# Kernel tuning notes

Measured on AMD Instinct MI355X. Metric: run time of the kernel, lower is better.

## Reference

```python
import jax, jax.numpy as jnp
import numpy as np

B, T, D_IN, D_OUT, H = 4, 2048, 768, 768, 12
HD = D_OUT // H  # 64


def setup_inputs() -> dict:
    key = jax.random.key(0)
    ks = jax.random.split(key, 6)
    s_in = 1.0 / np.sqrt(D_IN)
    s_out = 1.0 / np.sqrt(D_OUT)
    return {
        "x": jax.random.normal(ks[0], (B, T, D_IN), dtype=jnp.float32),
        "Wq": jax.random.uniform(ks[1], (D_IN, D_OUT), jnp.float32, -s_in, s_in),
        "Wk": jax.random.uniform(ks[2], (D_IN, D_OUT), jnp.float32, -s_in, s_in),
        "Wv": jax.random.uniform(ks[3], (D_IN, D_OUT), jnp.float32, -s_in, s_in),
        "Wo": jax.random.uniform(ks[4], (D_OUT, D_OUT), jnp.float32, -s_out, s_out),
        "bo": jax.random.uniform(ks[5], (D_OUT,), jnp.float32, -s_out, s_out),
    }


def reference(x, Wq, Wk, Wv, Wo, bo):
    b, t, _ = x.shape
    # QKV projections (no bias, per qkv_bias=False), split into heads: [b,h,t,hd]
    q = (x @ Wq).reshape(b, t, H, HD).transpose(0, 2, 1, 3)
    k = (x @ Wk).reshape(b, t, H, HD).transpose(0, 2, 1, 3)
    v = (x @ Wv).reshape(b, t, H, HD).transpose(0, 2, 1, 3)
    # NOTE: original calls masked_fill (non-in-place) and discards the result,
    # so NO causal mask is actually applied. Faithfully reproduce that.
    scores = jnp.einsum("bhqd,bhkd->bhqk", q, k)  # [b,h,t,t]
    attn = jax.nn.softmax(scores / jnp.sqrt(jnp.float32(HD)), axis=-1)
    # dropout p=0.0 (eval) -> identity
    ctx = jnp.einsum("bhqk,bhkd->bhqd", attn, v)  # [b,h,t,hd]
    ctx = ctx.transpose(0, 2, 1, 3).reshape(b, t, D_OUT)
    return ctx @ Wo + bo
```

## Files before the change

kernel.cpp:

```cpp
#include <hip/hip_runtime.h>
#include <hip/hip_bf16.h>
#include <stdint.h>


#define HH   12
#define TT   2048
#define DIN  768
#define DOUT 768
#define HD   64
#define BB   4
#define MTOT (BB*TT)
#define NQKV (3*DOUT)
#define QSCALE 0.1803368801111832f

typedef float  float4v  __attribute__((ext_vector_type(4)));
typedef float  float16v __attribute__((ext_vector_type(16)));
typedef __bf16 bf16x8   __attribute__((ext_vector_type(8)));
typedef short  short8v  __attribute__((ext_vector_type(8)));

#define AS1 __attribute__((address_space(1)))
#define AS3 __attribute__((address_space(3)))

static __device__ __forceinline__ void gload_lds16(const void* g, void* l) {
    __builtin_amdgcn_global_load_lds((AS1 void*)g, (AS3 void*)l, 16, 0, 0);
}

static __device__ __forceinline__ short f2bf(float f) {
    __bf16 h = (__bf16)f;
    return __builtin_bit_cast(short, h);
}

__global__ __launch_bounds__(256) void prep_kernel(const float* __restrict__ x,
                                                   const float* __restrict__ Wq,
                                                   const float* __restrict__ Wk,
                                                   const float* __restrict__ Wv,
                                                   const float* __restrict__ Wo,
                                                   short* __restrict__ Xb,
                                                   short* __restrict__ Wqkvt,
                                                   short* __restrict__ Wot) {
    __shared__ short tile[32 * 33];
    const int bz = blockIdx.z;
    if (bz == 4) {
        const int n4 = MTOT * DIN / 4;
        int i = (blockIdx.y * 24 + blockIdx.x) * 256 + threadIdx.x;
        for (; i < n4; i += 24 * 24 * 256) {
            float4 v = ((const float4*)x)[i];
            short4 o;
            o.x = f2bf(v.x); o.y = f2bf(v.y); o.z = f2bf(v.z); o.w = f2bf(v.w);
            ((short4*)Xb)[i] = o;
        }
        return;
    }
    const int bx = blockIdx.x, by = blockIdx.y;
    const float* W = (bz == 0) ? Wq : (bz == 1) ? Wk : (bz == 2) ? Wv : Wo;
    const int tx = threadIdx.x & 31, ty = threadIdx.x >> 5;
    for (int i = 0; i < 4; i++) {
        int k = by * 32 + ty + i * 8;
        tile[(ty + i * 8) * 33 + tx] = f2bf(W[(size_t)k * DOUT + bx * 32 + tx]);
    }
    __syncthreads();
    for (int i = 0; i < 4; i++) {
        int n = bx * 32 + ty + i * 8;
        int k = by * 32 + tx;
        short v = tile[tx * 33 + ty + i * 8];
        if (bz < 3) Wqkvt[(size_t)(bz * DOUT + n) * DIN + k] = v;
        else        Wot[(size_t)n * DOUT + k] = v;
    }
}

__global__ __launch_bounds__(256) void qkv_gemm_kernel(const short* __restrict__ Xb,
                                                       const short* __restrict__ Wt,
                                                       short* __restrict__ Qb,
                                                       short* __restrict__ Kb,
                                                       short* __restrict__ Vt) {
    __shared__ __align__(16) short lds[16384];
    short* ldsA = lds;
    short* ldsB = lds + 8192;
    const int t = threadIdx.x;
    const int w = t >> 6, lane = t & 63;
    const int quad = lane >> 4, l15 = lane & 15;
    const int m0 = blockIdx.x * 128, n0 = blockIdx.y * 128;
    const int wm = (w >> 1) * 64, wn = (w & 1) * 64;

    float4v acc[4][4];
    for (int i = 0; i < 4; i++)
        for (int j = 0; j < 4; j++)
            acc[i][j] = (float4v)0.0f;

    const int rA = t >> 3;
    const int cS = ((t & 7) ^ ((t >> 3) & 7)) * 8;
    const short* gA0 = Xb + (size_t)(m0 + rA) * DIN + cS;
    const short* gB0 = Wt + (size_t)(n0 + rA) * DIN + cS;

    for (int k0 = 0; k0 < DIN; k0 += 64) {
#pragma unroll
        for (int g = 0; g < 4; g++)
            gload_lds16(gA0 + (size_t)g * 32 * DIN + k0, &ldsA[(g * 256 + t) * 8]);
#pragma unroll
        for (int g = 0; g < 4; g++)
            gload_lds16(gB0 + (size_t)g * 32 * DIN + k0, &ldsB[(g * 256 + t) * 8]);
        __syncthreads();
#pragma unroll
        for (int kk = 0; kk < 2; kk++) {
            bf16x8 af[4], bfr[4];
            const int pos = ((kk * 4 + quad) ^ (l15 & 7)) * 8;
            for (int i = 0; i < 4; i++) af[i]  = *(const bf16x8*)&ldsA[(wm + i * 16 + l15) * 64 + pos];
            for (int j = 0; j < 4; j++) bfr[j] = *(const bf16x8*)&ldsB[(wn + j * 16 + l15) * 64 + pos];
            for (int i = 0; i < 4; i++)
                for (int j = 0; j < 4; j++)
                    acc[i][j] = __builtin_amdgcn_mfma_f32_16x16x32_bf16(af[i], bfr[j], acc[i][j], 0, 0, 0);
        }
        __syncthreads();
    }

    const int which = n0 / DOUT;
    if (which < 2) {
        short* ldsT = lds;
        const float sc = (which == 0) ? QSCALE : 1.0f;
        short* dst = (which == 0) ? Qb : Kb;
        const int n0sec = n0 - which * DOUT;
        for (int i = 0; i < 4; i++)
            for (int j = 0; j < 4; j++) {
                int col = wn + j * 16 + l15;
                int cx = col >> 3, co = col & 7;
                for (int r = 0; r < 4; r++) {
                    int row = wm + i * 16 + quad * 4 + r;
                    ldsT[row * 128 + ((cx ^ (row & 7)) * 8 + co)] = f2bf(acc[i][j][r] * sc);
                }
            }
        __syncthreads();
        for (int p = 0; p < 8; p++) {
            int row = p * 16 + (t >> 4);
            int cL = t & 15;
            short8v v = *(const short8v*)&ldsT[row * 128 + ((cL ^ (row & 7)) * 8)];
            int mg = m0 + row;
            int b2 = mg >> 11, tq = mg & 2047;
            int colg = n0sec + cL * 8;
            int hh = colg >> 6, d = colg & 63;
            *(short8v*)&dst[((size_t)((b2 * HH + hh) * TT + tq) << 6) + d] = v;
        }
    } else {
        short* ldsT = lds;
        const int n0r = n0 - 2 * DOUT;
        const int b = m0 >> 11, tq0 = m0 & 2047;
        for (int i = 0; i < 4; i++)
            for (int j = 0; j < 4; j++)
                for (int r = 0; r < 4; r++) {
                    int nl = wn + j * 16 + l15;
                    int ml = wm + i * 16 + quad * 4 + r;
                    int c = ml >> 3, o = ml & 7;
                    ldsT[nl * 128 + ((c ^ (nl & 7)) * 8 + o)] = f2bf(acc[i][j][r]);
                }
        __syncthreads();
        for (int p = 0; p < 8; p++) {
            int nrow = p * 16 + (t >> 4);
            int cc = t & 15;
            short8v v = *(const short8v*)&ldsT[nrow * 128 + ((cc ^ (nrow & 7)) * 8)];
            int colg = n0r + nrow;
            int hh = colg >> 6, d = colg & 63;
            *(short8v*)&Vt[(size_t)((b * HH + hh) * HD + d) * TT + tq0 + cc * 8] = v;
        }
    }
}

__global__ __launch_bounds__(256, 3) void attn_kernel(const short* __restrict__ Qb,
                                                      const short* __restrict__ Kb,
                                                      const short* __restrict__ Vt,
                                                      short* __restrict__ Ctx) {
    __shared__ __align__(16) short ldsK[2][64 * 64];
    __shared__ __align__(16) short ldsV[2][64 * 64];
    const int t = threadIdx.x;
    const int w = t >> 6, lane = t & 63;
    const int half = lane >> 5, m = lane & 31;
    const int bh = blockIdx.x;
    const int b = bh / HH, h = bh - b * HH;
    const int q0 = blockIdx.y * 128 + w * 32;

    const short* Qbase = Qb + (size_t)bh * TT * HD;
    const short* Kbase = Kb + (size_t)bh * TT * HD;
    const short* Vbase = Vt + (size_t)bh * HD * TT;

    bf16x8 qf[4];
#pragma unroll
    for (int s = 0; s < 4; s++)
        qf[s] = *(const bf16x8*)&Qbase[(q0 + m) * HD + s * 16 + half * 8];

    int kOff[2], vOff[2];
    {
        int r5 = t >> 3;
        int pi = ((r5 >> 3) & 1) * 16 + ((r5 >> 2) & 1) * 8 + ((r5 >> 4) & 1) * 4 + (r5 & 3);
#pragma unroll
        for (int g = 0; g < 2; g++) {
            kOff[g] = (g * 32 + pi) * 64 + (((t & 7) ^ (r5 & 7)) * 8);
            int vrow = g * 32 + r5;
            vOff[g] = vrow * TT + (((t & 7) ^ (vrow & 7)) * 8);
        }
    }

    auto stage = [&](int buf, int u0) {
#pragma unroll
        for (int g = 0; g < 2; g++)
            gload_lds16(Kbase + (size_t)u0 * 64 + kOff[g], &ldsK[buf][(g * 256 + t) * 8]);
#pragma unroll
        for (int g = 0; g < 2; g++)
            gload_lds16(Vbase + (size_t)u0 + vOff[g], &ldsV[buf][(g * 256 + t) * 8]);
    };

    float16v accO[2];
    accO[0] = (float16v)0.0f;
    accO[1] = (float16v)0.0f;
    float lsum = 0.0f;

    stage(0, 0);

    for (int it = 0; it < TT / 64; ++it) {
        __syncthreads();
        const int buf = it & 1;
        if (it + 1 < TT / 64) stage(buf ^ 1, (it + 1) * 64);
        const short* K_ = &ldsK[buf][0];
        const short* V_ = &ldsV[buf][0];

        float16v st0 = (float16v)0.0f;
        float16v st1 = (float16v)0.0f;
        __builtin_amdgcn_s_setprio(1);
#pragma unroll
        for (int s = 0; s < 4; s++) {
            bf16x8 ka = *(const bf16x8*)&K_[m * 64 + (((s * 2 + half) ^ (m & 7)) * 8)];
            st0 = __builtin_amdgcn_mfma_f32_32x32x16_bf16(ka, qf[s], st0, 0, 0, 0);
        }
#pragma unroll
        for (int s = 0; s < 4; s++) {
            bf16x8 ka = *(const bf16x8*)&K_[(32 + m) * 64 + (((s * 2 + half) ^ (m & 7)) * 8)];
            st1 = __builtin_amdgcn_mfma_f32_32x32x16_bf16(ka, qf[s], st1, 0, 0, 0);
        }
        __builtin_amdgcn_s_setprio(0);

        {
            float pe[16];
#pragma unroll
            for (int i = 0; i < 16; i++) pe[i] = __builtin_amdgcn_exp2f(st0[i]);
            bf16x8 ap[2];
#pragma unroll
            for (int i = 0; i < 4; i++) {
                ap[0][i]     = (__bf16)pe[i];
                ap[0][4 + i] = (__bf16)pe[8 + i];
                ap[1][i]     = (__bf16)pe[4 + i];
                ap[1][4 + i] = (__bf16)pe[12 + i];
            }
            __builtin_amdgcn_s_setprio(1);
#pragma unroll
            for (int ks = 0; ks < 2; ks++)
#pragma unroll
                for (int dt = 0; dt < 2; dt++) {
                    int row = dt * 32 + m;
                    bf16x8 bv = *(const bf16x8*)&V_[row * 64 + (((ks * 2 + half) ^ (row & 7)) * 8)];
                    accO[dt] = __builtin_amdgcn_mfma_f32_32x32x16_bf16(ap[ks], bv, accO[dt], 0, 0, 0);
                }
            __builtin_amdgcn_s_setprio(0);
            float ps[8];
#pragma unroll
            for (int i = 0; i < 8; i++) ps[i] = pe[i] + pe[i + 8];
#pragma unroll
            for (int i = 0; i < 4; i++) ps[i] += ps[i + 4];
            ps[0] += ps[2]; ps[1] += ps[3];
            lsum += ps[0] + ps[1];
        }

        {
            float pe[16];
#pragma unroll
            for (int i = 0; i < 16; i++) pe[i] = __builtin_amdgcn_exp2f(st1[i]);
            bf16x8 ap[2];
#pragma unroll
            for (int i = 0; i < 4; i++) {
                ap[0][i]     = (__bf16)pe[i];
                ap[0][4 + i] = (__bf16)pe[8 + i];
                ap[1][i]     = (__bf16)pe[4 + i];
                ap[1][4 + i] = (__bf16)pe[12 + i];
            }
            __builtin_amdgcn_s_setprio(1);
#pragma unroll
            for (int ks = 0; ks < 2; ks++)
#pragma unroll
                for (int dt = 0; dt < 2; dt++) {
                    int row = dt * 32 + m;
                    bf16x8 bv = *(const bf16x8*)&V_[row * 64 + (((4 + ks * 2 + half) ^ (row & 7)) * 8)];
                    accO[dt] = __builtin_amdgcn_mfma_f32_32x32x16_bf16(ap[ks], bv, accO[dt], 0, 0, 0);
                }
            __builtin_amdgcn_s_setprio(0);
            float ps[8];
#pragma unroll
            for (int i = 0; i < 8; i++) ps[i] = pe[i] + pe[i + 8];
#pragma unroll
            for (int i = 0; i < 4; i++) ps[i] += ps[i + 4];
            ps[0] += ps[2]; ps[1] += ps[3];
            lsum += ps[0] + ps[1];
        }
    }

    {
        float v = lsum + __shfl_xor(lsum, 32);
        float linv = 1.0f / v;
#pragma unroll
        for (int s = 0; s < 4; s++)
#pragma unroll
            for (int i = 0; i < 4; i++) {
                int reg = s * 4 + i;
                int qrow = i + s * 8 + half * 4;
                float ln = __shfl(linv, qrow);
                int qg = q0 + qrow;
                size_t base = (size_t)(b * TT + qg) * DOUT + h * HD + m;
                Ctx[base]      = f2bf(accO[0][reg] * ln);
                Ctx[base + 32] = f2bf(accO[1][reg] * ln);
            }
    }
}

__global__ __launch_bounds__(256) void out_gemm_kernel(const short* __restrict__ Cb,
                                                       const short* __restrict__ Wot,
                                                       const float* __restrict__ bo,
                                                       float* __restrict__ out) {
    __shared__ __align__(16) short ldsA[64 * 64];
    __shared__ __align__(16) short ldsB[128 * 64];
    const int t = threadIdx.x;
    const int w = t >> 6, lane = t & 63;
    const int quad = lane >> 4, l15 = lane & 15;
    const int m0 = blockIdx.x * 64, n0 = blockIdx.y * 128;
    const int wn = w * 32;

    float4v acc[4][2];
    for (int i = 0; i < 4; i++)
        for (int j = 0; j < 2; j++)
            acc[i][j] = (float4v)0.0f;

    const int rA = t >> 3;
    const int cS = ((t & 7) ^ ((t >> 3) & 7)) * 8;
    const short* gA0 = Cb + (size_t)(m0 + rA) * DOUT + cS;
    const short* gB0 = Wot + (size_t)(n0 + rA) * DOUT + cS;

    for (int k0 = 0; k0 < DOUT; k0 += 64) {
#pragma unroll
        for (int g = 0; g < 2; g++)
            gload_lds16(gA0 + (size_t)g * 32 * DOUT + k0, &ldsA[(g * 256 + t) * 8]);
#pragma unroll
        for (int g = 0; g < 4; g++)
            gload_lds16(gB0 + (size_t)g * 32 * DOUT + k0, &ldsB[(g * 256 + t) * 8]);
        __syncthreads();
#pragma unroll
        for (int kk = 0; kk < 2; kk++) {
            bf16x8 af[4], bfr[2];
            const int pos = ((kk * 4 + quad) ^ (l15 & 7)) * 8;
            for (int i = 0; i < 4; i++) af[i]  = *(const bf16x8*)&ldsA[(i * 16 + l15) * 64 + pos];
            for (int j = 0; j < 2; j++) bfr[j] = *(const bf16x8*)&ldsB[(wn + j * 16 + l15) * 64 + pos];
            for (int i = 0; i < 4; i++)
                for (int j = 0; j < 2; j++)
                    acc[i][j] = __builtin_amdgcn_mfma_f32_16x16x32_bf16(af[i], bfr[j], acc[i][j], 0, 0, 0);
        }
        __syncthreads();
    }

    for (int i = 0; i < 4; i++) {
        int m = m0 + i * 16 + quad * 4;
        for (int j = 0; j < 2; j++) {
            int n = n0 + wn + j * 16 + l15;
            float bias = bo[n];
            for (int r = 0; r < 4; r++)
                out[(size_t)(m + r) * DOUT + n] = acc[i][j][r] + bias;
        }
    }
}

extern "C" void kernel_launch(void* const* d_in, const int* in_sizes, int n_in,
                              void* d_out, int out_size, void* d_ws, size_t ws_size,
                              hipStream_t stream) {
    const float* x  = (const float*)d_in[0];
    const float* Wq = (const float*)d_in[1];
    const float* Wk = (const float*)d_in[2];
    const float* Wv = (const float*)d_in[3];
    const float* Wo = (const float*)d_in[4];
    const float* bo = (const float*)d_in[5];
    float* out = (float*)d_out;

    char* ws = (char*)d_ws;
    short* Xb    = (short*)(ws + 0);
    short* Wqkvt = (short*)(ws + 12582912);
    short* Wot   = (short*)(ws + 16121856);
    short* Qb    = (short*)(ws + 17301504);
    short* Kb    = (short*)(ws + 29884416);
    short* Vt    = (short*)(ws + 42467328);
    short* Cb    = (short*)(ws + 55050240);

    prep_kernel<<<dim3(24, 24, 5), 256, 0, stream>>>(x, Wq, Wk, Wv, Wo, Xb, Wqkvt, Wot);
    qkv_gemm_kernel<<<dim3(MTOT / 128, NQKV / 128), 256, 0, stream>>>(Xb, Wqkvt, Qb, Kb, Vt);
    attn_kernel<<<dim3(BB * HH, TT / 128), 256, 0, stream>>>(Qb, Kb, Vt, Cb);
    out_gemm_kernel<<<dim3(MTOT / 64, DOUT / 128), 256, 0, stream>>>(Cb, Wot, bo, out);
}
```

Baseline: 204.3 us.

## Double-buffer LDS tiles with K=32 steps in QKV and output GEMMs

Both projection GEMMs now stage K-slices of 32 into two alternating LDS buffers. The next slice's global-to-LDS loads are issued before computing on the current one, so only one barrier is needed per iteration. The aim is to hide global load latency behind MFMA work. The cost is twice as many iterations and barriers, plus a new XOR swizzle for the narrower rows that must stay free of bank conflicts.

```diff
diff --git a/kernel.cpp b/kernel.cpp
--- a/kernel.cpp
+++ b/kernel.cpp
@@ -74,8 +74,6 @@
                                                        short* __restrict__ Kb,
                                                        short* __restrict__ Vt) {
     __shared__ __align__(16) short lds[16384];
-    short* ldsA = lds;
-    short* ldsB = lds + 8192;
     const int t = threadIdx.x;
     const int w = t >> 6, lane = t & 63;
     const int quad = lane >> 4, l15 = lane & 15;
@@ -87,31 +85,34 @@
         for (int j = 0; j < 4; j++)
             acc[i][j] = (float4v)0.0f;
 
-    const int rA = t >> 3;
-    const int cS = ((t & 7) ^ ((t >> 3) & 7)) * 8;
-    const short* gA0 = Xb + (size_t)(m0 + rA) * DIN + cS;
-    const short* gB0 = Wt + (size_t)(n0 + rA) * DIN + cS;
-
-    for (int k0 = 0; k0 < DIN; k0 += 64) {
-#pragma unroll
-        for (int g = 0; g < 4; g++)
-            gload_lds16(gA0 + (size_t)g * 32 * DIN + k0, &ldsA[(g * 256 + t) * 8]);
-#pragma unroll
-        for (int g = 0; g < 4; g++)
-            gload_lds16(gB0 + (size_t)g * 32 * DIN + k0, &ldsB[(g * 256 + t) * 8]);
-        __syncthreads();
-#pragma unroll
-        for (int kk = 0; kk < 2; kk++) {
-            bf16x8 af[4], bfr[4];
-            const int pos = ((kk * 4 + quad) ^ (l15 & 7)) * 8;
-            for (int i = 0; i < 4; i++) af[i]  = *(const bf16x8*)&ldsA[(wm + i * 16 + l15) * 64 + pos];
-            for (int j = 0; j < 4; j++) bfr[j] = *(const bf16x8*)&ldsB[(wn + j * 16 + l15) * 64 + pos];
-            for (int i = 0; i < 4; i++)
-                for (int j = 0; j < 4; j++)
-                    acc[i][j] = __builtin_amdgcn_mfma_f32_16x16x32_bf16(af[i], bfr[j], acc[i][j], 0, 0, 0);
-        }
-        __syncthreads();
-    }
+    const int rA = t >> 2;
+    const int cSw = ((t & 3) ^ ((t >> 3) & 3)) * 8;
+    const short* gA0 = Xb + (size_t)(m0 + rA) * DIN + cSw;
+    const short* gB0 = Wt + (size_t)(n0 + rA) * DIN + cSw;
+    const int pos = (quad ^ ((l15 >> 1) & 3)) * 8;
+
+    auto stage = [&](int buf, int k0) {
+        int off = buf << 13;
+        gload_lds16(gA0 + k0,            &lds[off + t * 8]);
+        gload_lds16(gA0 + 64 * DIN + k0, &lds[off + (t + 256) * 8]);
+        gload_lds16(gB0 + k0,            &lds[off + 4096 + t * 8]);
+        gload_lds16(gB0 + 64 * DIN + k0, &lds[off + 4096 + (t + 256) * 8]);
+    };
+
+    stage(0, 0);
+    for (int it = 0; it < DIN / 32; ++it) {
+        __syncthreads();
+        if (it + 1 < DIN / 32) stage((it & 1) ^ 1, (it + 1) * 32);
+        const short* A_ = lds + ((it & 1) << 13);
+        const short* B_ = A_ + 4096;
+        bf16x8 af[4], bfr[4];
+        for (int i = 0; i < 4; i++) af[i]  = *(const bf16x8*)&A_[(wm + i * 16 + l15) * 32 + pos];
+        for (int j = 0; j < 4; j++) bfr[j] = *(const bf16x8*)&B_[(wn + j * 16 + l15) * 32 + pos];
+        for (int i = 0; i < 4; i++)
+            for (int j = 0; j < 4; j++)
+                acc[i][j] = __builtin_amdgcn_mfma_f32_16x16x32_bf16(af[i], bfr[j], acc[i][j], 0, 0, 0);
+    }
+    __syncthreads();
 
     const int which = n0 / DOUT;
     if (which < 2) {
@@ -320,8 +321,7 @@
                                                        const short* __restrict__ Wot,
                                                        const float* __restrict__ bo,
                                                        float* __restrict__ out) {
-    __shared__ __align__(16) short ldsA[64 * 64];
-    __shared__ __align__(16) short ldsB[128 * 64];
+    __shared__ __align__(16) short lds[12288];
     const int t = threadIdx.x;
     const int w = t >> 6, lane = t & 63;
     const int quad = lane >> 4, l15 = lane & 15;
@@ -333,30 +333,31 @@
         for (int j = 0; j < 2; j++)
             acc[i][j] = (float4v)0.0f;
 
-    const int rA = t >> 3;
-    const int cS = ((t & 7) ^ ((t >> 3) & 7)) * 8;
-    const short* gA0 = Cb + (size_t)(m0 + rA) * DOUT + cS;
-    const short* gB0 = Wot + (size_t)(n0 + rA) * DOUT + cS;
-
-    for (int k0 = 0; k0 < DOUT; k0 += 64) {
-#pragma unroll
-        for (int g = 0; g < 2; g++)
-            gload_lds16(gA0 + (size_t)g * 32 * DOUT + k0, &ldsA[(g * 256 + t) * 8]);
-#pragma unroll
-        for (int g = 0; g < 4; g++)
-            gload_lds16(gB0 + (size_t)g * 32 * DOUT + k0, &ldsB[(g * 256 + t) * 8]);
-        __syncthreads();
-#pragma unroll
-        for (int kk = 0; kk < 2; kk++) {
-            bf16x8 af[4], bfr[2];
-            const int pos = ((kk * 4 + quad) ^ (l15 & 7)) * 8;
-            for (int i = 0; i < 4; i++) af[i]  = *(const bf16x8*)&ldsA[(i * 16 + l15) * 64 + pos];
-            for (int j = 0; j < 2; j++) bfr[j] = *(const bf16x8*)&ldsB[(wn + j * 16 + l15) * 64 + pos];
-            for (int i = 0; i < 4; i++)
-                for (int j = 0; j < 2; j++)
-                    acc[i][j] = __builtin_amdgcn_mfma_f32_16x16x32_bf16(af[i], bfr[j], acc[i][j], 0, 0, 0);
-        }
-        __syncthreads();
+    const int rA = t >> 2;
+    const int cSw = ((t & 3) ^ ((t >> 3) & 3)) * 8;
+    const short* gA0 = Cb + (size_t)(m0 + rA) * DOUT + cSw;
+    const short* gB0 = Wot + (size_t)(n0 + rA) * DOUT + cSw;
+    const int pos = (quad ^ ((l15 >> 1) & 3)) * 8;
+
+    auto stage = [&](int buf, int k0) {
+        int off = buf * 6144;
+        gload_lds16(gA0 + k0,             &lds[off + t * 8]);
+        gload_lds16(gB0 + k0,             &lds[off + 2048 + t * 8]);
+        gload_lds16(gB0 + 64 * DOUT + k0, &lds[off + 2048 + (t + 256) * 8]);
+    };
+
+    stage(0, 0);
+    for (int it = 0; it < DOUT / 32; ++it) {
+        __syncthreads();
+        if (it + 1 < DOUT / 32) stage((it & 1) ^ 1, (it + 1) * 32);
+        const short* A_ = lds + (it & 1) * 6144;
+        const short* B_ = A_ + 2048;
+        bf16x8 af[4], bfr[2];
+        for (int i = 0; i < 4; i++) af[i]  = *(const bf16x8*)&A_[(i * 16 + l15) * 32 + pos];
+        for (int j = 0; j < 2; j++) bfr[j] = *(const bf16x8*)&B_[(wn + j * 16 + l15) * 32 + pos];
+        for (int i = 0; i < 4; i++)
+            for (int j = 0; j < 2; j++)
+                acc[i][j] = __builtin_amdgcn_mfma_f32_16x16x32_bf16(af[i], bfr[j], acc[i][j], 0, 0, 0);
     }
 
     for (int i = 0; i < 4; i++) {
```

Measured after the change: 207.4 us. About the same (+1.5%).
